# Optimization experiments

Measured on AMD Instinct MI355X. Metric: run time of the kernel, lower is better.

Reference implementation:

```python
import jax, jax.numpy as jnp
import numpy as np

N = 50000       # num_nodes
R = 8           # num_relations
H = 64          # hidden_channels
C = 16          # num_classes
E = 1_600_000   # num edges (avg degree 32)
T = 8192        # number of 'author' target nodes (first T nodes after to_homogeneous)


def setup_inputs() -> dict:
    key = jax.random.key(0)
    ks = jax.random.split(key, 12)
    s = 0.02
    return {
        "edge_index": jax.random.randint(ks[0], (2, E), 0, N),
        "edge_type": jax.random.randint(ks[1], (E,), 0, R),
        "num_target": T,
        # conv1 (featureless: weight is an embedding table [R, N, H], root is [N, H])
        "weight1": jax.random.normal(ks[2], (R, N, H), jnp.float32) * s,
        "root1": jax.random.normal(ks[3], (N, H), jnp.float32) * s,
        "bias1": jnp.zeros((H,), jnp.float32),
        # conv2
        "weight2": jax.random.normal(ks[4], (R, H, H), jnp.float32) * s,
        "root2": jax.random.normal(ks[5], (H, H), jnp.float32) * s,
        "bias2": jnp.zeros((H,), jnp.float32),
        # linear head
        "lin_w": jax.random.normal(ks[6], (H, C), jnp.float32) * s,
        "lin_b": jnp.zeros((C,), jnp.float32),
    }


def reference(edge_index, edge_type, num_target, weight1, root1, bias1,
              weight2, root2, bias2, lin_w, lin_b):
    src, dst = edge_index[0], edge_index[1]
    E_ = src.shape[0]

    # PyG RGCNConv aggregates with MEAN per relation, then sums over relations.
    # Count edges per (dst node, relation) to form the per-relation mean denominator.
    seg = dst * R + edge_type                          # [E] combined (node, relation) id
    cnt = jax.ops.segment_sum(jnp.ones((E_,), jnp.float32), seg, num_segments=N * R)
    scale = (1.0 / jnp.maximum(cnt, 1.0))[seg]         # [E]

    # ---- conv1: x is None -> message = weight1[edge_type][src] (embedding lookup) ----
    m1 = weight1[edge_type, src] * scale[:, None]      # [E, H]
    h1 = jax.ops.segment_sum(m1, dst, num_segments=N)  # [N, H]
    h1 = h1 + root1 + bias1                            # root1[arange(N)] == root1
    h1 = jax.nn.elu(h1)

    # ---- conv2: message = h1[src] @ weight2[edge_type] ----
    # Precompute per-relation node transforms [R, N, H], then gather per edge.
    hr = jnp.einsum('nh,rhk->rnk', h1, weight2)        # [R, N, H]
    m2 = hr[edge_type, src] * scale[:, None]           # [E, H]
    h2 = jax.ops.segment_sum(m2, dst, num_segments=N)  # [N, H]
    h2 = h2 + h1 @ root2 + bias2
    h2 = jax.nn.elu(h2)

    # ---- linear head on the target ('author') node slice ----
    out = h2[:num_target] @ lin_w + lin_b              # [T, C]
    return out
```

## Files before the change

kernel.cpp:

```cpp
#include <hip/hip_runtime.h>

#define NNODES 50000
#define NREL   8
#define HID    64
#define NCLS   16
#define NEDGE  1600000
#define NTGT   8192
#define NBINS  (NNODES * NREL)
#define CHUNK  1024
#define NCHUNK ((NBINS + CHUNK - 1) / CHUNK)

__device__ __forceinline__ float elu1(float x) { return x > 0.f ? x : expm1f(x); }

__global__ void count_kernel(const int* __restrict__ ei, const int* __restrict__ et,
                             int* __restrict__ cnt, int* __restrict__ epos) {
  int e4 = (blockIdx.x * blockDim.x + threadIdx.x) * 4;
  if (e4 >= NEDGE) return;
  int4 d = *(const int4*)(ei + NEDGE + e4);
  int4 r = *(const int4*)(et + e4);
  int4 p;
  p.x = atomicAdd(&cnt[d.x * NREL + r.x], 1);
  p.y = atomicAdd(&cnt[d.y * NREL + r.y], 1);
  p.z = atomicAdd(&cnt[d.z * NREL + r.z], 1);
  p.w = atomicAdd(&cnt[d.w * NREL + r.w], 1);
  *(int4*)(epos + e4) = p;
}

__global__ void chunk_sum_kernel(const int* __restrict__ cnt, int* __restrict__ csum) {
  __shared__ int sw[4];
  int t = threadIdx.x, lane = t & 63, wid = t >> 6;
  int i = blockIdx.x * CHUNK + t * 4;
  int s = 0;
  if (i < NBINS) { int4 c = *(const int4*)(cnt + i); s = c.x + c.y + c.z + c.w; }
#pragma unroll
  for (int off = 32; off >= 1; off >>= 1) s += __shfl_xor(s, off);
  if (lane == 0) sw[wid] = s;
  __syncthreads();
  if (t == 0) csum[blockIdx.x] = sw[0] + sw[1] + sw[2] + sw[3];
}

__global__ void scan_csum_kernel(const int* __restrict__ csum, int* __restrict__ cbase) {
  __shared__ int sw[8];
  int t = threadIdx.x, lane = t & 63, wid = t >> 6;
  int v0 = (t < NCHUNK) ? csum[t] : 0;
  int v = v0;
#pragma unroll
  for (int off = 1; off < 64; off <<= 1) {
    int u = __shfl_up(v, off);
    if (lane >= off) v += u;
  }
  if (lane == 63) sw[wid] = v;
  __syncthreads();
  if (t == 0) {
    int run = 0;
#pragma unroll
    for (int j = 0; j < 8; ++j) { int x = sw[j]; sw[j] = run; run += x; }
  }
  __syncthreads();
  if (t < NCHUNK) cbase[t] = sw[wid] + (v - v0);
}

__global__ void scan_write_kernel(const int* __restrict__ cnt, const int* __restrict__ cbase,
                                  int* __restrict__ binptr) {
  __shared__ int sw[4];
  int t = threadIdx.x, lane = t & 63, wid = t >> 6;
  int i = blockIdx.x * CHUNK + t * 4;
  int4 c = make_int4(0, 0, 0, 0);
  if (i < NBINS) c = *(const int4*)(cnt + i);
  int p0 = c.x, p1 = p0 + c.y, p2 = p1 + c.z, s = p2 + c.w;
  int v = s;
#pragma unroll
  for (int off = 1; off < 64; off <<= 1) {
    int u = __shfl_up(v, off);
    if (lane >= off) v += u;
  }
  if (lane == 63) sw[wid] = v;
  __syncthreads();
  if (t == 0) {
    int run = 0;
#pragma unroll
    for (int j = 0; j < 4; ++j) { int x = sw[j]; sw[j] = run; run += x; }
  }
  __syncthreads();
  if (i < NBINS) {
    int excl = cbase[blockIdx.x] + sw[wid] + (v - s);
    *(int4*)(binptr + i) = make_int4(excl, excl + p0, excl + p1, excl + p2);
  }
  if (blockIdx.x == 0 && t == 0) binptr[NBINS] = NEDGE;
}

__global__ void scatter_kernel(const int* __restrict__ ei, const int* __restrict__ et,
                               const int* __restrict__ epos, const int* __restrict__ binptr,
                               int2* __restrict__ epo) {
  int e4 = (blockIdx.x * blockDim.x + threadIdx.x) * 4;
  if (e4 >= NEDGE) return;
  int4 sv = *(const int4*)(ei + e4);
  int4 dv = *(const int4*)(ei + NEDGE + e4);
  int4 rv = *(const int4*)(et + e4);
  int4 pv = *(const int4*)(epos + e4);
  int srcs[4] = {sv.x, sv.y, sv.z, sv.w};
  int dsts[4] = {dv.x, dv.y, dv.z, dv.w};
  int rels[4] = {rv.x, rv.y, rv.z, rv.w};
  int poss[4] = {pv.x, pv.y, pv.z, pv.w};
#pragma unroll
  for (int j = 0; j < 4; ++j) {
    int bin = dsts[j] * NREL + rels[j];
    int b = binptr[bin];
    int c = binptr[bin + 1] - b;
    float sc = 1.0f / (float)c;
    epo[b + poss[j]] = make_int2(rels[j] * NNODES + srcs[j], __float_as_int(sc));
  }
}

__global__ __launch_bounds__(256) void conv1_kernel(
    const int* __restrict__ binptr, const int2* __restrict__ epo,
    const float* __restrict__ w1, const float* __restrict__ root1,
    const float* __restrict__ bias1, float* __restrict__ h1) {
  int wave = blockIdx.x * 4 + (threadIdx.x >> 6);
  if (wave >= NNODES) return;
  int lane = threadIdx.x & 63;
  int b0 = binptr[wave * NREL], b8 = binptr[wave * NREL + NREL];
  float acc = 0.f;
  for (int eb = b0; eb < b8; eb += 64) {
    int mb = min(64, b8 - eb);
    int2 q = epo[eb + min(lane, mb - 1)];
    int j = 0;
    for (; j + 8 <= mb; j += 8) {
      float a[8], sc[8];
#pragma unroll
      for (int u = 0; u < 8; ++u) {
        int idx = __builtin_amdgcn_readlane(q.x, j + u);
        sc[u] = __int_as_float(__builtin_amdgcn_readlane(q.y, j + u));
        a[u] = w1[(((size_t)(unsigned)idx) << 6) + lane];
      }
#pragma unroll
      for (int u = 0; u < 8; ++u) acc = fmaf(a[u], sc[u], acc);
    }
    for (; j < mb; ++j) {
      int idx = __builtin_amdgcn_readlane(q.x, j);
      float s = __int_as_float(__builtin_amdgcn_readlane(q.y, j));
      acc = fmaf(w1[(((size_t)(unsigned)idx) << 6) + lane], s, acc);
    }
  }
  float v = acc + root1[(wave << 6) + lane] + bias1[lane];
  h1[(wave << 6) + lane] = elu1(v);
}

__global__ __launch_bounds__(256) void conv2a_kernel(
    const int* __restrict__ binptr, const int2* __restrict__ epo,
    const float* __restrict__ h1, float* __restrict__ agg, int nodeBase, int nloc) {
  int wv = blockIdx.x * 4 + (threadIdx.x >> 6);
  if (wv >= nloc * NREL) return;
  int lane = threadIdx.x & 63;
  int r = wv & 7;
  int bin = (nodeBase + (wv >> 3)) * NREL + r;
  int bb = binptr[bin], ee = binptr[bin + 1];
  int rb = r * NNODES;
  float s = 0.f;
  for (int e = bb; e < ee; e += 64) {
    int mb = min(64, ee - e);
    int2 q = epo[e + min(lane, mb - 1)];
    int j = 0;
    for (; j + 4 <= mb; j += 4) {
      float a[4];
#pragma unroll
      for (int u = 0; u < 4; ++u) {
        int i0 = __builtin_amdgcn_readlane(q.x, j + u) - rb;
        a[u] = h1[(((size_t)(unsigned)i0) << 6) + lane];
      }
#pragma unroll
      for (int u = 0; u < 4; ++u) s += a[u];
    }
    for (; j < mb; ++j) {
      int i0 = __builtin_amdgcn_readlane(q.x, j) - rb;
      s += h1[(((size_t)(unsigned)i0) << 6) + lane];
    }
  }
  float out = (ee > bb) ? s * (1.0f / (float)(ee - bb)) : 0.f;
  agg[((size_t)wv << 6) + lane] = out;
}

__global__ __launch_bounds__(256, 4) void conv2b_kernel(
    const float* __restrict__ agg, const float* __restrict__ h1,
    const float* __restrict__ w2, const float* __restrict__ root2,
    const float* __restrict__ bias2, float* __restrict__ h2, int nodeBase) {
  __shared__ float sW[HID * HID];
  int t = threadIdx.x, lane = t & 63, wid = t >> 6;
  int ln0 = blockIdx.x * 8 + wid * 2;
  float bz = bias2[lane];
  float o0 = bz, o1 = bz;
  for (int r = 0; r < NREL; ++r) {
    if (r) __syncthreads();
#pragma unroll
    for (int i = 0; i < 4; ++i)
      *(float4*)(sW + t * 4 + i * 1024) = *(const float4*)(w2 + (r << 12) + t * 4 + i * 1024);
    __syncthreads();
    const float* a0 = agg + (((size_t)((ln0 + 0) * NREL + r)) << 6);
    const float* a1 = agg + (((size_t)((ln0 + 1) * NREL + r)) << 6);
#pragma unroll 16
    for (int k = 0; k < HID; ++k) {
      float w = sW[(k << 6) + lane];
      o0 = fmaf(a0[k], w, o0);
      o1 = fmaf(a1[k], w, o1);
    }
  }
  __syncthreads();
#pragma unroll
  for (int i = 0; i < 4; ++i)
    *(float4*)(sW + t * 4 + i * 1024) = *(const float4*)(root2 + t * 4 + i * 1024);
  __syncthreads();
  int g0 = nodeBase + ln0;
  const float* r0p = h1 + ((size_t)(g0 + 0) << 6);
  const float* r1p = h1 + ((size_t)(g0 + 1) << 6);
#pragma unroll 16
  for (int k = 0; k < HID; ++k) {
    float w = sW[(k << 6) + lane];
    o0 = fmaf(r0p[k], w, o0);
    o1 = fmaf(r1p[k], w, o1);
  }
  h2[((size_t)(g0 + 0) << 6) + lane] = elu1(o0);
  h2[((size_t)(g0 + 1) << 6) + lane] = elu1(o1);
}

__global__ void head_kernel(const float* __restrict__ h2, const float* __restrict__ lin_w,
                            const float* __restrict__ lin_b, float* __restrict__ out) {
  int t = blockIdx.x * blockDim.x + threadIdx.x;
  if (t >= NTGT * NCLS) return;
  int n = t >> 4, c = t & 15;
  float acc = lin_b[c];
#pragma unroll
  for (int k = 0; k < HID; ++k)
    acc = fmaf(h2[(n << 6) + k], lin_w[k * NCLS + c], acc);
  out[t] = acc;
}

extern "C" void kernel_launch(void* const* d_in, const int* in_sizes, int n_in,
                              void* d_out, int out_size, void* d_ws, size_t ws_size,
                              hipStream_t stream) {
  const int*   ei    = (const int*)d_in[0];
  const int*   et    = (const int*)d_in[1];
  const float* w1    = (const float*)d_in[3];
  const float* root1 = (const float*)d_in[4];
  const float* bias1 = (const float*)d_in[5];
  const float* w2    = (const float*)d_in[6];
  const float* root2 = (const float*)d_in[7];
  const float* bias2 = (const float*)d_in[8];
  const float* lin_w = (const float*)d_in[9];
  const float* lin_b = (const float*)d_in[10];
  float* out = (float*)d_out;

  char* ws = (char*)d_ws;
  float* h1     = (float*)ws;
  int*   cnt    = (int*)ws;
  int*   epos   = (int*)(ws + (size_t)NBINS * 4);
  char*  p      = ws + (size_t)NNODES * HID * 4;
  int*   binptr = (int*)p;  p += ((size_t)(NBINS + 1) * 4 + 255) & ~(size_t)255;
  int*   csum   = (int*)p;  p += ((size_t)NCHUNK * 4 + 255) & ~(size_t)255;
  int*   cbase  = (int*)p;  p += ((size_t)NCHUNK * 4 + 255) & ~(size_t)255;
  int2*  epo    = (int2*)p; p += (size_t)NEDGE * 8;
  float* h2     = (float*)p; p += (size_t)NTGT * HID * 4;
  float* agg    = (float*)p;
  size_t fixed  = (size_t)(p - ws);
  int chunk = (fixed + (size_t)NTGT * NREL * HID * 4 <= ws_size) ? NTGT : NTGT / 2;

  hipMemsetAsync(cnt, 0, (size_t)NBINS * sizeof(int), stream);
  count_kernel<<<(NEDGE / 4 + 255) / 256, 256, 0, stream>>>(ei, et, cnt, epos);
  chunk_sum_kernel<<<NCHUNK, 256, 0, stream>>>(cnt, csum);
  scan_csum_kernel<<<1, 512, 0, stream>>>(csum, cbase);
  scan_write_kernel<<<NCHUNK, 256, 0, stream>>>(cnt, cbase, binptr);
  scatter_kernel<<<(NEDGE / 4 + 255) / 256, 256, 0, stream>>>(ei, et, epos, binptr, epo);
  conv1_kernel<<<(NNODES + 3) / 4, 256, 0, stream>>>(binptr, epo, w1, root1, bias1, h1);
  for (int c = 0; c < NTGT / chunk; ++c) {
    conv2a_kernel<<<(chunk * NREL) / 4, 256, 0, stream>>>(binptr, epo, h1, agg, c * chunk, chunk);
    conv2b_kernel<<<chunk / 8, 256, 0, stream>>>(agg, h1, w2, root2, bias2, h2, c * chunk);
  }
  head_kernel<<<(NTGT * NCLS + 255) / 256, 256, 0, stream>>>(h2, lin_w, lin_b, out);
}
```

Baseline: 402.1 us.

## Fuse head into conv2b, move scatter atomics, widen conv1 unroll, adaptive chunking

The linear head is folded into conv2b through wave reductions, which removes the h2 buffer and one kernel launch. Edge slot assignment moves from count_kernel's returned atomic positions to a fill-pointer atomic in the scatter kernel, so the epos array is no longer written or read. The conv1 gather unroll grows from 8 to 16 with a 4-wide tail loop to keep more loads in flight. The conv2 chunk size is now picked adaptively from the workspace size. Risks: the ordering inside each bin becomes nondeterministic, and the head adds 32 wave reductions per wave.

```diff
diff --git a/kernel.cpp b/kernel.cpp
--- a/kernel.cpp
+++ b/kernel.cpp
@@ -12,18 +12,22 @@
 
 __device__ __forceinline__ float elu1(float x) { return x > 0.f ? x : expm1f(x); }
 
+__device__ __forceinline__ float wave_sum(float v) {
+#pragma unroll
+  for (int off = 32; off; off >>= 1) v += __shfl_xor(v, off);
+  return v;
+}
+
 __global__ void count_kernel(const int* __restrict__ ei, const int* __restrict__ et,
-                             int* __restrict__ cnt, int* __restrict__ epos) {
+                             int* __restrict__ cnt) {
   int e4 = (blockIdx.x * blockDim.x + threadIdx.x) * 4;
   if (e4 >= NEDGE) return;
   int4 d = *(const int4*)(ei + NEDGE + e4);
   int4 r = *(const int4*)(et + e4);
-  int4 p;
-  p.x = atomicAdd(&cnt[d.x * NREL + r.x], 1);
-  p.y = atomicAdd(&cnt[d.y * NREL + r.y], 1);
-  p.z = atomicAdd(&cnt[d.z * NREL + r.z], 1);
-  p.w = atomicAdd(&cnt[d.w * NREL + r.w], 1);
-  *(int4*)(epos + e4) = p;
+  atomicAdd(&cnt[d.x * NREL + r.x], 1);
+  atomicAdd(&cnt[d.y * NREL + r.y], 1);
+  atomicAdd(&cnt[d.z * NREL + r.z], 1);
+  atomicAdd(&cnt[d.w * NREL + r.w], 1);
 }
 
 __global__ void chunk_sum_kernel(const int* __restrict__ cnt, int* __restrict__ csum) {
@@ -61,7 +65,7 @@
 }
 
 __global__ void scan_write_kernel(const int* __restrict__ cnt, const int* __restrict__ cbase,
-                                  int* __restrict__ binptr) {
+                                  int* __restrict__ binptr, int* __restrict__ fill) {
   __shared__ int sw[4];
   int t = threadIdx.x, lane = t & 63, wid = t >> 6;
   int i = blockIdx.x * CHUNK + t * 4;
@@ -84,31 +88,30 @@
   __syncthreads();
   if (i < NBINS) {
     int excl = cbase[blockIdx.x] + sw[wid] + (v - s);
-    *(int4*)(binptr + i) = make_int4(excl, excl + p0, excl + p1, excl + p2);
+    int4 o = make_int4(excl, excl + p0, excl + p1, excl + p2);
+    *(int4*)(binptr + i) = o;
+    *(int4*)(fill + i) = o;
   }
   if (blockIdx.x == 0 && t == 0) binptr[NBINS] = NEDGE;
 }
 
 __global__ void scatter_kernel(const int* __restrict__ ei, const int* __restrict__ et,
-                               const int* __restrict__ epos, const int* __restrict__ binptr,
+                               const int* __restrict__ cnt, int* __restrict__ fill,
                                int2* __restrict__ epo) {
   int e4 = (blockIdx.x * blockDim.x + threadIdx.x) * 4;
   if (e4 >= NEDGE) return;
   int4 sv = *(const int4*)(ei + e4);
   int4 dv = *(const int4*)(ei + NEDGE + e4);
   int4 rv = *(const int4*)(et + e4);
-  int4 pv = *(const int4*)(epos + e4);
   int srcs[4] = {sv.x, sv.y, sv.z, sv.w};
   int dsts[4] = {dv.x, dv.y, dv.z, dv.w};
   int rels[4] = {rv.x, rv.y, rv.z, rv.w};
-  int poss[4] = {pv.x, pv.y, pv.z, pv.w};
 #pragma unroll
   for (int j = 0; j < 4; ++j) {
     int bin = dsts[j] * NREL + rels[j];
-    int b = binptr[bin];
-    int c = binptr[bin + 1] - b;
-    float sc = 1.0f / (float)c;
-    epo[b + poss[j]] = make_int2(rels[j] * NNODES + srcs[j], __float_as_int(sc));
+    int c = cnt[bin];
+    int pos = atomicAdd(&fill[bin], 1);
+    epo[pos] = make_int2(rels[j] * NNODES + srcs[j], __float_as_int(1.0f / (float)c));
   }
 }
 
@@ -125,16 +128,27 @@
     int mb = min(64, b8 - eb);
     int2 q = epo[eb + min(lane, mb - 1)];
     int j = 0;
-    for (; j + 8 <= mb; j += 8) {
-      float a[8], sc[8];
-#pragma unroll
-      for (int u = 0; u < 8; ++u) {
+    for (; j + 16 <= mb; j += 16) {
+      float a[16], sc[16];
+#pragma unroll
+      for (int u = 0; u < 16; ++u) {
         int idx = __builtin_amdgcn_readlane(q.x, j + u);
         sc[u] = __int_as_float(__builtin_amdgcn_readlane(q.y, j + u));
         a[u] = w1[(((size_t)(unsigned)idx) << 6) + lane];
       }
 #pragma unroll
-      for (int u = 0; u < 8; ++u) acc = fmaf(a[u], sc[u], acc);
+      for (int u = 0; u < 16; ++u) acc = fmaf(a[u], sc[u], acc);
+    }
+    for (; j + 4 <= mb; j += 4) {
+      float a[4], sc[4];
+#pragma unroll
+      for (int u = 0; u < 4; ++u) {
+        int idx = __builtin_amdgcn_readlane(q.x, j + u);
+        sc[u] = __int_as_float(__builtin_amdgcn_readlane(q.y, j + u));
+        a[u] = w1[(((size_t)(unsigned)idx) << 6) + lane];
+      }
+#pragma unroll
+      for (int u = 0; u < 4; ++u) acc = fmaf(a[u], sc[u], acc);
     }
     for (; j < mb; ++j) {
       int idx = __builtin_amdgcn_readlane(q.x, j);
@@ -183,7 +197,8 @@
 __global__ __launch_bounds__(256, 4) void conv2b_kernel(
     const float* __restrict__ agg, const float* __restrict__ h1,
     const float* __restrict__ w2, const float* __restrict__ root2,
-    const float* __restrict__ bias2, float* __restrict__ h2, int nodeBase) {
+    const float* __restrict__ bias2, const float* __restrict__ lin_w,
+    const float* __restrict__ lin_b, float* __restrict__ out, int nodeBase) {
   __shared__ float sW[HID * HID];
   int t = threadIdx.x, lane = t & 63, wid = t >> 6;
   int ln0 = blockIdx.x * 8 + wid * 2;
@@ -218,20 +233,26 @@
     o0 = fmaf(r0p[k], w, o0);
     o1 = fmaf(r1p[k], w, o1);
   }
-  h2[((size_t)(g0 + 0) << 6) + lane] = elu1(o0);
-  h2[((size_t)(g0 + 1) << 6) + lane] = elu1(o1);
-}
-
-__global__ void head_kernel(const float* __restrict__ h2, const float* __restrict__ lin_w,
-                            const float* __restrict__ lin_b, float* __restrict__ out) {
-  int t = blockIdx.x * blockDim.x + threadIdx.x;
-  if (t >= NTGT * NCLS) return;
-  int n = t >> 4, c = t & 15;
-  float acc = lin_b[c];
-#pragma unroll
-  for (int k = 0; k < HID; ++k)
-    acc = fmaf(h2[(n << 6) + k], lin_w[k * NCLS + c], acc);
-  out[t] = acc;
+  o0 = elu1(o0);
+  o1 = elu1(o1);
+  float lw[16];
+#pragma unroll
+  for (int c4 = 0; c4 < 4; ++c4) {
+    float4 v = *(const float4*)(lin_w + lane * NCLS + c4 * 4);
+    lw[c4 * 4 + 0] = v.x; lw[c4 * 4 + 1] = v.y; lw[c4 * 4 + 2] = v.z; lw[c4 * 4 + 3] = v.w;
+  }
+  float res0 = 0.f, res1 = 0.f;
+#pragma unroll
+  for (int c = 0; c < NCLS; ++c) {
+    float s0 = wave_sum(o0 * lw[c]);
+    float s1 = wave_sum(o1 * lw[c]);
+    if (lane == c) { res0 = s0; res1 = s1; }
+  }
+  if (lane < NCLS) {
+    float lb = lin_b[lane];
+    out[(size_t)(g0 + 0) * NCLS + lane] = res0 + lb;
+    out[(size_t)(g0 + 1) * NCLS + lane] = res1 + lb;
+  }
 }
 
 extern "C" void kernel_launch(void* const* d_in, const int* in_sizes, int n_in,
@@ -252,27 +273,27 @@
   char* ws = (char*)d_ws;
   float* h1     = (float*)ws;
   int*   cnt    = (int*)ws;
-  int*   epos   = (int*)(ws + (size_t)NBINS * 4);
   char*  p      = ws + (size_t)NNODES * HID * 4;
   int*   binptr = (int*)p;  p += ((size_t)(NBINS + 1) * 4 + 255) & ~(size_t)255;
+  int*   fill   = (int*)p;  p += ((size_t)NBINS * 4 + 255) & ~(size_t)255;
   int*   csum   = (int*)p;  p += ((size_t)NCHUNK * 4 + 255) & ~(size_t)255;
   int*   cbase  = (int*)p;  p += ((size_t)NCHUNK * 4 + 255) & ~(size_t)255;
   int2*  epo    = (int2*)p; p += (size_t)NEDGE * 8;
-  float* h2     = (float*)p; p += (size_t)NTGT * HID * 4;
   float* agg    = (float*)p;
   size_t fixed  = (size_t)(p - ws);
-  int chunk = (fixed + (size_t)NTGT * NREL * HID * 4 <= ws_size) ? NTGT : NTGT / 2;
+  int chunk = 1024;
+  for (int c = NTGT; c >= 2048; c >>= 1)
+    if (fixed + (size_t)c * NREL * HID * 4 <= ws_size) { chunk = c; break; }
 
   hipMemsetAsync(cnt, 0, (size_t)NBINS * sizeof(int), stream);
-  count_kernel<<<(NEDGE / 4 + 255) / 256, 256, 0, stream>>>(ei, et, cnt, epos);
+  count_kernel<<<(NEDGE / 4 + 255) / 256, 256, 0, stream>>>(ei, et, cnt);
   chunk_sum_kernel<<<NCHUNK, 256, 0, stream>>>(cnt, csum);
   scan_csum_kernel<<<1, 512, 0, stream>>>(csum, cbase);
-  scan_write_kernel<<<NCHUNK, 256, 0, stream>>>(cnt, cbase, binptr);
-  scatter_kernel<<<(NEDGE / 4 + 255) / 256, 256, 0, stream>>>(ei, et, epos, binptr, epo);
+  scan_write_kernel<<<NCHUNK, 256, 0, stream>>>(cnt, cbase, binptr, fill);
+  scatter_kernel<<<(NEDGE / 4 + 255) / 256, 256, 0, stream>>>(ei, et, cnt, fill, epo);
   conv1_kernel<<<(NNODES + 3) / 4, 256, 0, stream>>>(binptr, epo, w1, root1, bias1, h1);
   for (int c = 0; c < NTGT / chunk; ++c) {
     conv2a_kernel<<<(chunk * NREL) / 4, 256, 0, stream>>>(binptr, epo, h1, agg, c * chunk, chunk);
-    conv2b_kernel<<<chunk / 8, 256, 0, stream>>>(agg, h1, w2, root2, bias2, h2, c * chunk);
-  }
-  head_kernel<<<(NTGT * NCLS + 255) / 256, 256, 0, stream>>>(h2, lin_w, lin_b, out);
-}
+    conv2b_kernel<<<chunk / 8, 256, 0, stream>>>(agg, h1, w2, root2, bias2, lin_w, lin_b, out, c * chunk);
+  }
+}
```

Result: slower. 446.2 us (+11.0%).
